# Performance work log

Measured on AMD Instinct MI355X. Metric: run time of the kernel, lower is better.

Reference implementation:

```python
import jax, jax.numpy as jnp
from jax import lax
import numpy as np

L, B, E, D, V, MID = 128, 32, 512, 1024, 32000, 4


def sru_layer(x, c0, W, b, use_tanh=True):
    """One SRU layer. x: (L,B,n_in), c0: (B,n_out), W: (n_in, k*n_out), b: (2*n_out)."""
    n_out = c0.shape[-1]
    k = W.shape[1] // n_out
    U = jnp.einsum('lbi,io->lbo', x, W)  # parallel GEMM over all timesteps
    x_tilde = U[..., :n_out]
    f = jax.nn.sigmoid(U[..., n_out:2 * n_out] + b[:n_out])
    r = jax.nn.sigmoid(U[..., 2 * n_out:3 * n_out] + b[n_out:])
    hw = U[..., 3 * n_out:] if k == 4 else x  # highway path

    def step(c, fx):
        f_t, xt_t = fx
        c = f_t * c + (1.0 - f_t) * xt_t
        return c, c

    c_last, cs = lax.scan(step, c0, (f, x_tilde))
    g = jnp.tanh(cs) if use_tanh else cs
    h = r * g + (1.0 - r) * hw
    return h, c_last


def setup_inputs() -> dict:
    key = jax.random.key(0)
    ks = jax.random.split(key, 8)
    s_e = (3.0 / E) ** 0.5
    s_d = (3.0 / D) ** 0.5
    return {
        'x': jax.random.randint(ks[0], (L, B), 0, V, dtype=jnp.int64),
        'c1': jnp.zeros((B, D), jnp.float32),
        'c2': jnp.zeros((MID, B, D), jnp.float32),
        'c3': jnp.zeros((B, E), jnp.float32),
        'emb': jax.random.uniform(ks[1], (V, E), jnp.float32, -s_d, s_d),
        'out_bias': jnp.zeros((V,), jnp.float32),
        'W1': jax.random.uniform(ks[2], (E, 4 * D), jnp.float32, -s_e, s_e),
        'b1': jnp.zeros((2 * D,), jnp.float32),
        'W2': jax.random.uniform(ks[3], (MID, D, 3 * D), jnp.float32, -s_d, s_d),
        'b2': jnp.zeros((MID, 2 * D), jnp.float32),
        'W3': jax.random.uniform(ks[4], (D, 4 * E), jnp.float32, -s_d, s_d),
        'b3': jnp.zeros((2 * E,), jnp.float32),
    }


def reference(x, c1, c2, c3, emb, out_bias, W1, b1, W2, b2, W3, b3):
    h = emb[x]  # (L,B,E) embedding lookup (dropout=0 in eval)
    h, _ = sru_layer(h, c1, W1, b1)            # E -> D (k=4)
    for i in range(W2.shape[0]):               # D -> D stacked (k=3)
        h, _ = sru_layer(h, c2[i], W2[i], b2[i])
    h, _ = sru_layer(h, c3, W3, b3)            # D -> E (k=4)
    logits = h.reshape(-1, E) @ emb.T + out_bias  # tied-weight projection (L*B, V)
    return logits
```

## Files before the change

### kernel.cpp

```cpp
#include <hip/hip_runtime.h>


typedef __attribute__((ext_vector_type(8))) __bf16 bf16x8;
typedef __attribute__((ext_vector_type(4))) float f32x4;
typedef __attribute__((ext_vector_type(4))) float float4v;
typedef __attribute__((ext_vector_type(4))) unsigned short u16x4;

__device__ __forceinline__ unsigned short f2bf(float f) {
  unsigned int u = __builtin_bit_cast(unsigned int, f);
  u += 0x7fffu + ((u >> 16) & 1u);
  return (unsigned short)(u >> 16);
}
__device__ __forceinline__ float bf2f(unsigned short v) {
  unsigned int u = ((unsigned int)v) << 16;
  return __builtin_bit_cast(float, u);
}

#define GLDS16(SRC, DST)                                                      \
  __builtin_amdgcn_global_load_lds(                                           \
      (__attribute__((address_space(1))) void*)(SRC),                         \
      (__attribute__((address_space(3))) void*)(DST), 16, 0, 0)

template <bool BF16OUT, bool GATHER>
__global__ __launch_bounds__(256, 4)
void gemm128(const unsigned short* __restrict__ A,
             const unsigned short* __restrict__ B,
             void* __restrict__ Cv, const float* __restrict__ bias,
             const int* __restrict__ xrow,
             int M, int N, int K, int tiles_m) {
  __shared__ __align__(16) unsigned short As[128 * 64];
  __shared__ __align__(16) unsigned short Bs[128 * 64];
  __shared__ int xs[128];

  const int tid  = threadIdx.x;
  const int lane = tid & 63;
  const int wave = tid >> 6;
  const int wm = wave >> 1, wn = wave & 1;

  const int nwg  = gridDim.x;
  const int orig = blockIdx.x;
  const int wg   = (orig & 7) * (nwg >> 3) + (orig >> 3);
  const int by = wg % tiles_m, bx = wg / tiles_m;
  const int m0 = by * 128, n0 = bx * 128;

  if constexpr (GATHER) {
    if (tid < 128) xs[tid] = xrow[m0 + tid];
    __syncthreads();
  }

  const int srow  = lane >> 3;
  const int sslot = (lane & 7) ^ srow;
  const int fr = lane & 15;
  const int s0 = (lane >> 4) ^ (lane & 7);
  const int lg = lane >> 4;

  f32x4 acc[4][4] = {};

  const int ksteps = K >> 6;
  for (int ks = 0; ks < ksteps; ++ks) {
    const int k0 = ks << 6;
#pragma unroll
    for (int j = 0; j < 4; ++j) {
      const int rbase = (j * 4 + wave) * 8;
      const int r = rbase + srow;
      const unsigned short* sa;
      if constexpr (GATHER)
        sa = A + (size_t)xs[r] * K + k0 + sslot * 8;
      else
        sa = A + (size_t)(m0 + r) * K + k0 + sslot * 8;
      const unsigned short* sb = B + (size_t)(n0 + r) * K + k0 + sslot * 8;
      GLDS16(sa, &As[rbase * 64]);
      GLDS16(sb, &Bs[rbase * 64]);
    }
    __syncthreads();
#pragma unroll
    for (int kk = 0; kk < 2; ++kk) {
      const int slot = s0 ^ (kk << 2);
      bf16x8 a[4], b[4];
#pragma unroll
      for (int m = 0; m < 4; ++m)
        a[m] = *(const bf16x8*)&As[(wm * 64 + m * 16 + fr) * 64 + slot * 8];
#pragma unroll
      for (int n = 0; n < 4; ++n)
        b[n] = *(const bf16x8*)&Bs[(wn * 64 + n * 16 + fr) * 64 + slot * 8];
#pragma unroll
      for (int m = 0; m < 4; ++m)
#pragma unroll
        for (int n = 0; n < 4; ++n)
          acc[m][n] = __builtin_amdgcn_mfma_f32_16x16x32_bf16(a[m], b[n],
                                                              acc[m][n], 0, 0, 0);
    }
    __syncthreads();
  }

  if constexpr (BF16OUT) {
    unsigned short* C = (unsigned short*)Cv;
#pragma unroll
    for (int m = 0; m < 4; ++m) {
      const int row = m0 + wm * 64 + m * 16 + lg * 4;
#pragma unroll
      for (int r = 0; r < 4; ++r) {
        unsigned short* Crow = C + (size_t)(row + r) * N + n0 + wn * 64 + fr;
#pragma unroll
        for (int n = 0; n < 4; ++n)
          Crow[n * 16] = f2bf(acc[m][n][r]);
      }
    }
  } else {
    float* C = (float*)Cv;
    float bv[4];
#pragma unroll
    for (int n = 0; n < 4; ++n)
      bv[n] = bias ? bias[n0 + wn * 64 + n * 16 + fr] : 0.0f;
#pragma unroll
    for (int m = 0; m < 4; ++m) {
      const int row = m0 + wm * 64 + m * 16 + lg * 4;
#pragma unroll
      for (int r = 0; r < 4; ++r) {
        float* Crow = C + (size_t)(row + r) * N + n0 + wn * 64 + fr;
#pragma unroll
        for (int n = 0; n < 4; ++n)
          __builtin_nontemporal_store(acc[m][n][r] + bv[n], &Crow[n * 16]);
      }
    }
  }
}

template <bool K4>
__global__ void scan_k(const unsigned short* __restrict__ U,
                       const float* __restrict__ bias,
                       const float* __restrict__ c0,
                       const unsigned short* __restrict__ hin,
                       unsigned short* __restrict__ hout, int n_out) {
  const int idx = blockIdx.x * 64 + threadIdx.x;
  const int b = idx / n_out;
  const int d = idx - b * n_out;
  const float biasf = bias[d];
  const float biasr = bias[n_out + d];
  float c = c0[idx];
  const int rowlen = (K4 ? 4 : 3) * n_out;
  const unsigned short* Up = U + (size_t)b * rowlen + d;
  const size_t lstride = (size_t)32 * rowlen;
  const unsigned short* hp = hin + (size_t)b * n_out + d;
  unsigned short* op = hout + (size_t)b * n_out + d;
  const size_t hstride = (size_t)32 * n_out;

  float xt0, fr0, rr0, hw0, xt1, fr1, rr1, hw1;
  float xt2, fr2, rr2, hw2, xt3, fr3, rr3, hw3;

#define SRU_LOAD(S)                                                           \
  do {                                                                        \
    xt##S = bf2f(Up[0]);                                                      \
    fr##S = bf2f(Up[n_out]);                                                  \
    rr##S = bf2f(Up[2 * n_out]);                                              \
    hw##S = K4 ? bf2f(Up[3 * n_out]) : bf2f(*hp);                             \
    Up += lstride;                                                            \
    hp += hstride;                                                            \
  } while (0)

#define SRU_STEP(S)                                                           \
  do {                                                                        \
    const float f = 1.0f / (1.0f + __expf(-(fr##S + biasf)));                 \
    const float r = 1.0f / (1.0f + __expf(-(rr##S + biasr)));                 \
    c = f * c + (1.0f - f) * xt##S;                                           \
    const float e2 = __expf(2.0f * c);                                        \
    const float g = 1.0f - 2.0f / (e2 + 1.0f);                                \
    *op = f2bf(r * g + (1.0f - r) * hw##S);                                   \
    op += hstride;                                                            \
  } while (0)

  SRU_LOAD(0); SRU_LOAD(1); SRU_LOAD(2); SRU_LOAD(3);
  for (int l = 0; l < 124; l += 4) {
    SRU_STEP(0); SRU_LOAD(0);
    SRU_STEP(1); SRU_LOAD(1);
    SRU_STEP(2); SRU_LOAD(2);
    SRU_STEP(3); SRU_LOAD(3);
  }
  SRU_STEP(0); SRU_STEP(1); SRU_STEP(2); SRU_STEP(3);
#undef SRU_LOAD
#undef SRU_STEP
}

__device__ __forceinline__ void transpose_tile64(const float* __restrict__ W,
                                                 unsigned short* __restrict__ Wt,
                                                 int K, int N, int bx, int by,
                                                 int tid) {
  __shared__ float tile[64][65];
  const int n0 = bx * 64, k0 = by * 64;
  const int tx = tid & 63, ty = tid >> 6;
#pragma unroll
  for (int i = 0; i < 64; i += 4)
    tile[ty + i][tx] = W[(size_t)(k0 + ty + i) * N + n0 + tx];
  __syncthreads();
#pragma unroll
  for (int i = 0; i < 64; i += 4)
    Wt[(size_t)(n0 + ty + i) * K + k0 + tx] = f2bf(tile[tx][ty + i]);
}

__global__ void prep_k(const float* __restrict__ emb,
                       const float* __restrict__ W1,
                       const float* __restrict__ W2,
                       const float* __restrict__ W3,
                       unsigned short* __restrict__ embbf,
                       unsigned short* __restrict__ W1t,
                       unsigned short* __restrict__ W2t,
                       unsigned short* __restrict__ W3t) {
  const int blk = blockIdx.x;
  const int tid = threadIdx.x;
  if (blk < 16000) {
    const int i = blk * 256 + tid;
    const float4v v = ((const float4v*)emb)[i];
    u16x4 o;
    o.x = f2bf(v.x); o.y = f2bf(v.y); o.z = f2bf(v.z); o.w = f2bf(v.w);
    ((u16x4*)embbf)[i] = o;
  } else if (blk < 16512) {
    const int r = blk - 16000;
    transpose_tile64(W1, W1t, 512, 4096, r & 63, r >> 6, tid);
  } else if (blk < 19584) {
    const int r = blk - 16512;
    const int i = r / 768, rr = r - i * 768;
    transpose_tile64(W2 + (size_t)i * 3145728, W2t + (size_t)i * 3145728,
                     1024, 3072, rr % 48, rr / 48, tid);
  } else {
    const int r = blk - 19584;
    transpose_tile64(W3, W3t, 1024, 2048, r & 31, r >> 5, tid);
  }
}

extern "C" void kernel_launch(void* const* d_in, const int* in_sizes, int n_in,
                              void* d_out, int out_size, void* d_ws, size_t ws_size,
                              hipStream_t stream) {
  (void)in_sizes; (void)n_in; (void)out_size; (void)ws_size;
  const int*   x     = (const int*)d_in[0];
  const float* c1    = (const float*)d_in[1];
  const float* c2    = (const float*)d_in[2];
  const float* c3    = (const float*)d_in[3];
  const float* emb   = (const float*)d_in[4];
  const float* obias = (const float*)d_in[5];
  const float* W1    = (const float*)d_in[6];
  const float* b1    = (const float*)d_in[7];
  const float* W2    = (const float*)d_in[8];
  const float* b2    = (const float*)d_in[9];
  const float* W3    = (const float*)d_in[10];
  const float* b3    = (const float*)d_in[11];

  char* ws = (char*)d_ws;
  unsigned short* hbfA  = (unsigned short*)ws;
  unsigned short* hbfB  = (unsigned short*)(ws + 8388608);
  unsigned short* embbf = (unsigned short*)(ws + 16777216);
  unsigned short* W1t   = (unsigned short*)(ws + 49545216);
  unsigned short* W2t   = (unsigned short*)(ws + 53739520);
  unsigned short* W3t   = (unsigned short*)(ws + 78905344);
  unsigned short* U = (unsigned short*)d_out;

  prep_k<<<20096, 256, 0, stream>>>(emb, W1, W2, W3, embbf, W1t, W2t, W3t);

  gemm128<true, true><<<1024, 256, 0, stream>>>(embbf, W1t, U, nullptr, x,
                                                4096, 4096, 512, 32);
  scan_k<true><<<512, 64, 0, stream>>>(U, b1, c1, hbfB, hbfB, 1024);

  const unsigned short* hin = hbfB;
  unsigned short* hout = hbfA;
  for (int i = 0; i < 4; ++i) {
    gemm128<true, false><<<768, 256, 0, stream>>>(hin, W2t + (size_t)i * 3145728,
                                                  U, nullptr, nullptr,
                                                  4096, 3072, 1024, 32);
    scan_k<false><<<512, 64, 0, stream>>>(U, b2 + i * 2048, c2 + (size_t)i * 32768,
                                          hin, hout, 1024);
    const unsigned short* t = hin; hin = hout; hout = (unsigned short*)t;
  }

  gemm128<true, false><<<512, 256, 0, stream>>>(hin, W3t, U, nullptr, nullptr,
                                                4096, 2048, 1024, 32);
  scan_k<true><<<256, 64, 0, stream>>>(U, b3, c3, hout, hout, 512);

  gemm128<false, false><<<8000, 256, 0, stream>>>(hout, embbf, (float*)d_out,
                                                  obias, nullptr,
                                                  4096, 32000, 512, 32);
}
```

Baseline: 544.3 us.

## Split SRU scan over time into four chunks with a two-pass affine combine

The recurrence scan is parallelised along the time axis. Each block now runs four waves, and each wave handles 32 of the 128 timesteps for the same 64 channels. In the first pass each wave computes the affine composition (product of f, accumulated term) over its chunk and stores it in LDS. After a barrier, each wave folds in the earlier chunks' maps to get its starting c and then replays its chunk to produce outputs. This cuts the serial dependency chain per thread and multiplies the number of active waves on the device, at the cost of reading f and x_tilde twice and recomputing the sigmoid.

```diff
diff --git a/kernel.cpp b/kernel.cpp
--- a/kernel.cpp
+++ b/kernel.cpp
@@ -127,58 +127,91 @@
 }
 
 template <bool K4>
-__global__ void scan_k(const unsigned short* __restrict__ U,
-                       const float* __restrict__ bias,
-                       const float* __restrict__ c0,
-                       const unsigned short* __restrict__ hin,
-                       unsigned short* __restrict__ hout, int n_out) {
-  const int idx = blockIdx.x * 64 + threadIdx.x;
+__global__ __launch_bounds__(256)
+void scan_k(const unsigned short* __restrict__ U,
+            const float* __restrict__ bias,
+            const float* __restrict__ c0v,
+            const unsigned short* __restrict__ hin,
+            unsigned short* __restrict__ hout, int n_out) {
+  __shared__ float lA[4][64], lB[4][64];
+  const int lane = threadIdx.x & 63;
+  const int ch   = threadIdx.x >> 6;
+  const int idx  = blockIdx.x * 64 + lane;
   const int b = idx / n_out;
   const int d = idx - b * n_out;
   const float biasf = bias[d];
   const float biasr = bias[n_out + d];
-  float c = c0[idx];
   const int rowlen = (K4 ? 4 : 3) * n_out;
-  const unsigned short* Up = U + (size_t)b * rowlen + d;
   const size_t lstride = (size_t)32 * rowlen;
-  const unsigned short* hp = hin + (size_t)b * n_out + d;
-  unsigned short* op = hout + (size_t)b * n_out + d;
   const size_t hstride = (size_t)32 * n_out;
-
-  float xt0, fr0, rr0, hw0, xt1, fr1, rr1, hw1;
-  float xt2, fr2, rr2, hw2, xt3, fr3, rr3, hw3;
-
-#define SRU_LOAD(S)                                                           \
-  do {                                                                        \
-    xt##S = bf2f(Up[0]);                                                      \
-    fr##S = bf2f(Up[n_out]);                                                  \
-    rr##S = bf2f(Up[2 * n_out]);                                              \
-    hw##S = K4 ? bf2f(Up[3 * n_out]) : bf2f(*hp);                             \
-    Up += lstride;                                                            \
-    hp += hstride;                                                            \
-  } while (0)
-
-#define SRU_STEP(S)                                                           \
-  do {                                                                        \
-    const float f = 1.0f / (1.0f + __expf(-(fr##S + biasf)));                 \
-    const float r = 1.0f / (1.0f + __expf(-(rr##S + biasr)));                 \
-    c = f * c + (1.0f - f) * xt##S;                                           \
-    const float e2 = __expf(2.0f * c);                                        \
-    const float g = 1.0f - 2.0f / (e2 + 1.0f);                                \
-    *op = f2bf(r * g + (1.0f - r) * hw##S);                                   \
-    op += hstride;                                                            \
-  } while (0)
-
-  SRU_LOAD(0); SRU_LOAD(1); SRU_LOAD(2); SRU_LOAD(3);
-  for (int l = 0; l < 124; l += 4) {
-    SRU_STEP(0); SRU_LOAD(0);
-    SRU_STEP(1); SRU_LOAD(1);
-    SRU_STEP(2); SRU_LOAD(2);
-    SRU_STEP(3); SRU_LOAD(3);
-  }
-  SRU_STEP(0); SRU_STEP(1); SRU_STEP(2); SRU_STEP(3);
-#undef SRU_LOAD
-#undef SRU_STEP
+  const unsigned short* Up0 = U + (size_t)b * rowlen + d + (size_t)(ch * 32) * lstride;
+
+  float A = 1.0f, Bv = 0.0f;
+  {
+    const unsigned short* p = Up0;
+    float xt0, fr0, xt1, fr1, xt2, fr2, xt3, fr3;
+#define P1_LOAD(S)                                                            \
+    do { xt##S = bf2f(p[0]); fr##S = bf2f(p[n_out]); p += lstride; } while (0)
+#define P1_STEP(S)                                                            \
+    do {                                                                      \
+      const float f = 1.0f / (1.0f + __expf(-(fr##S + biasf)));               \
+      A *= f;  Bv = f * Bv + (1.0f - f) * xt##S;                              \
+    } while (0)
+    P1_LOAD(0); P1_LOAD(1); P1_LOAD(2); P1_LOAD(3);
+    for (int s = 0; s < 28; s += 4) {
+      P1_STEP(0); P1_LOAD(0);
+      P1_STEP(1); P1_LOAD(1);
+      P1_STEP(2); P1_LOAD(2);
+      P1_STEP(3); P1_LOAD(3);
+    }
+    P1_STEP(0); P1_STEP(1); P1_STEP(2); P1_STEP(3);
+#undef P1_LOAD
+#undef P1_STEP
+  }
+  lA[ch][lane] = A;
+  lB[ch][lane] = Bv;
+  __syncthreads();
+
+  float c = c0v[idx];
+  for (int i = 0; i < ch; ++i)
+    c = lA[i][lane] * c + lB[i][lane];
+
+  {
+    const unsigned short* p = Up0;
+    const unsigned short* hp = hin + (size_t)b * n_out + d + (size_t)(ch * 32) * hstride;
+    unsigned short* op = hout + (size_t)b * n_out + d + (size_t)(ch * 32) * hstride;
+    float xt0, fr0, rr0, hw0, xt1, fr1, rr1, hw1;
+    float xt2, fr2, rr2, hw2, xt3, fr3, rr3, hw3;
+#define P2_LOAD(S)                                                            \
+    do {                                                                      \
+      xt##S = bf2f(p[0]);                                                     \
+      fr##S = bf2f(p[n_out]);                                                 \
+      rr##S = bf2f(p[2 * n_out]);                                             \
+      hw##S = K4 ? bf2f(p[3 * n_out]) : bf2f(*hp);                            \
+      p += lstride;                                                           \
+      hp += hstride;                                                          \
+    } while (0)
+#define P2_STEP(S)                                                            \
+    do {                                                                      \
+      const float f = 1.0f / (1.0f + __expf(-(fr##S + biasf)));               \
+      const float r = 1.0f / (1.0f + __expf(-(rr##S + biasr)));               \
+      c = f * c + (1.0f - f) * xt##S;                                         \
+      const float e2 = __expf(2.0f * c);                                      \
+      const float g = 1.0f - 2.0f / (e2 + 1.0f);                              \
+      *op = f2bf(r * g + (1.0f - r) * hw##S);                                 \
+      op += hstride;                                                          \
+    } while (0)
+    P2_LOAD(0); P2_LOAD(1); P2_LOAD(2); P2_LOAD(3);
+    for (int s = 0; s < 28; s += 4) {
+      P2_STEP(0); P2_LOAD(0);
+      P2_STEP(1); P2_LOAD(1);
+      P2_STEP(2); P2_LOAD(2);
+      P2_STEP(3); P2_LOAD(3);
+    }
+    P2_STEP(0); P2_STEP(1); P2_STEP(2); P2_STEP(3);
+#undef P2_LOAD
+#undef P2_STEP
+  }
 }
 
 __device__ __forceinline__ void transpose_tile64(const float* __restrict__ W,
@@ -257,7 +290,7 @@
 
   gemm128<true, true><<<1024, 256, 0, stream>>>(embbf, W1t, U, nullptr, x,
                                                 4096, 4096, 512, 32);
-  scan_k<true><<<512, 64, 0, stream>>>(U, b1, c1, hbfB, hbfB, 1024);
+  scan_k<true><<<512, 256, 0, stream>>>(U, b1, c1, hbfB, hbfB, 1024);
 
   const unsigned short* hin = hbfB;
   unsigned short* hout = hbfA;
@@ -265,14 +298,14 @@
     gemm128<true, false><<<768, 256, 0, stream>>>(hin, W2t + (size_t)i * 3145728,
                                                   U, nullptr, nullptr,
                                                   4096, 3072, 1024, 32);
-    scan_k<false><<<512, 64, 0, stream>>>(U, b2 + i * 2048, c2 + (size_t)i * 32768,
-                                          hin, hout, 1024);
+    scan_k<false><<<512, 256, 0, stream>>>(U, b2 + i * 2048, c2 + (size_t)i * 32768,
+                                           hin, hout, 1024);
     const unsigned short* t = hin; hin = hout; hout = (unsigned short*)t;
   }
 
   gemm128<true, false><<<512, 256, 0, stream>>>(hin, W3t, U, nullptr, nullptr,
                                                 4096, 2048, 1024, 32);
-  scan_k<true><<<256, 64, 0, stream>>>(U, b3, c3, hout, hout, 512);
+  scan_k<true><<<256, 256, 0, stream>>>(U, b3, c3, hout, hout, 512);
 
   gemm128<false, false><<<8000, 256, 0, stream>>>(hout, embbf, (float*)d_out,
                                                   obias, nullptr,
```

Result: faster. 463.3 us (-14.9%).
